# Kernel optimization log

Hardware: AMD Instinct MI355X
Metric: run time of the kernel (lower is better)

Reference implementation:

```python
import jax, jax.numpy as jnp
import numpy as np

N_NODES = 50000
N_EDGES = 800000
NODE_DIM = 64
EDGE_DIM = 16
HID = 64
HEADS = 4
LAYERS = 3
N_GRAPHS = 32
N_QUERY = 4096
BN_EPS = 1e-5
LRELU_SLOPE = 0.2


def setup_inputs() -> dict:
    key = jax.random.key(0)
    ks = jax.random.split(key, 20)
    s = 0.1  # weight scale
    return {
        "node_feat": jax.random.normal(ks[0], (N_NODES, NODE_DIM), jnp.float32),
        "edge_feat": jax.random.normal(ks[1], (N_EDGES, EDGE_DIM), jnp.float32),
        "node_proj_w": jax.random.normal(ks[2], (NODE_DIM, HID), jnp.float32) * s,
        "node_proj_b": jax.random.normal(ks[3], (HID,), jnp.float32) * s,
        "edge_proj_w": jax.random.normal(ks[4], (EDGE_DIM, HID), jnp.float32) * s,
        "edge_proj_b": jax.random.normal(ks[5], (HID,), jnp.float32) * s,
        "fc_w": jax.random.normal(ks[6], (LAYERS, HID, HEADS * HID), jnp.float32) * s,
        "fc_edge_w": jax.random.normal(ks[7], (LAYERS, HID, HEADS * HID), jnp.float32) * s,
        "attn_l": jax.random.normal(ks[8], (LAYERS, HEADS, HID), jnp.float32) * s,
        "attn_r": jax.random.normal(ks[9], (LAYERS, HEADS, HID), jnp.float32) * s,
        "attn_e": jax.random.normal(ks[10], (LAYERS, HEADS, HID), jnp.float32) * s,
        "conv_bias": jax.random.normal(ks[11], (LAYERS, HEADS * HID), jnp.float32) * s,
        "bn_gamma": jnp.ones((LAYERS, HID), jnp.float32),
        "bn_beta": jnp.zeros((LAYERS, HID), jnp.float32),
        "head_w": jax.random.normal(ks[12], (HEADS * HID, HID), jnp.float32) * s,
        "head_b": jax.random.normal(ks[13], (HID,), jnp.float32) * s,
        "src": jax.random.randint(ks[14], (N_EDGES,), 0, N_NODES, jnp.int64 if jax.config.jax_enable_x64 else jnp.int32),
        "dst": jax.random.randint(ks[15], (N_EDGES,), 0, N_NODES, jnp.int64 if jax.config.jax_enable_x64 else jnp.int32),
        "graph_ids": jnp.sort(jax.random.randint(ks[16], (N_NODES,), 0, N_GRAPHS)),
        "nodes_idx": jax.random.randint(ks[17], (N_QUERY,), 0, N_NODES),
        "num_graphs": N_GRAPHS,
    }


def reference(node_feat, edge_feat, node_proj_w, node_proj_b, edge_proj_w,
              edge_proj_b, fc_w, fc_edge_w, attn_l, attn_r, attn_e, conv_bias,
              bn_gamma, bn_beta, head_w, head_b, src, dst, graph_ids,
              nodes_idx, num_graphs):
    N = node_feat.shape[0]
    L, H, D = attn_l.shape

    nodes = node_feat @ node_proj_w + node_proj_b        # (N, hid)
    edges = edge_feat @ edge_proj_w + edge_proj_b        # (E, hid)

    x = None
    for l in range(L):
        # NOTE: faithful to original -- every layer consumes the ORIGINAL
        # projected node features (output is never fed back into `nodes`).
        ft = (nodes @ fc_w[l]).reshape(N, H, D)          # (N, H, D)
        fe = (edges @ fc_edge_w[l]).reshape(-1, H, D)    # (E, H, D)
        el = jnp.einsum('nhd,hd->nh', ft, attn_l[l])     # (N, H)
        er = jnp.einsum('nhd,hd->nh', ft, attn_r[l])
        ee = jnp.einsum('ehd,hd->eh', fe, attn_e[l])     # (E, H)
        e = jax.nn.leaky_relu(el[src] + er[dst] + ee, LRELU_SLOPE)
        # edge softmax over incoming edges of each destination node
        emax = jax.ops.segment_max(e, dst, num_segments=N)
        ex = jnp.exp(e - emax[dst])
        denom = jax.ops.segment_sum(ex, dst, num_segments=N)
        a = ex / denom[dst]                              # (E, H)
        # message = a * (feat_src + feat_edge), scatter-sum to dst
        m = a[:, :, None] * (ft[src] + fe)               # (E, H, D)
        rst = jax.ops.segment_sum(m, dst, num_segments=N)  # (N, H, D)
        rst = jax.nn.silu(rst + conv_bias[l].reshape(H, D))
        # BatchNorm1d(hidden) after permute(0,2,1): channel dim is D,
        # stats over (N, H). Training-mode batch statistics.
        mean = rst.mean(axis=(0, 1))
        var = rst.var(axis=(0, 1))
        x = (rst - mean) * jax.lax.rsqrt(var + BN_EPS) * bn_gamma[l] + bn_beta[l]

    x = x.reshape(N, H * D) @ head_w + head_b            # (N, hid)

    ones = jnp.ones((N, 1), x.dtype)
    sums = jax.ops.segment_sum(x, graph_ids, num_segments=num_graphs)
    counts = jax.ops.segment_sum(ones, graph_ids, num_segments=num_graphs)
    pooled = sums / jnp.maximum(counts, 1.0)             # (G, hid)
    return pooled, x[nodes_idx]
```

## Files before the change

### kernel.cpp

```cpp
#include <hip/hip_runtime.h>
#include <cstdint>
#include <cstddef>

#define N_NODES 50000
#define N_EDGES 800000
#define HID 64
#define HEADS 4
#define N_GRAPHS 32
#define N_QUERY 4096
#define N_TILES 3125
#define N_CWAVES 1563
#define N_CBLK 391
#define N_SBLK 49

typedef unsigned short ushort_t;
typedef unsigned int uint_t;
typedef __attribute__((ext_vector_type(8))) short short8_t;
typedef __attribute__((ext_vector_type(4))) float f32x4_t;

__device__ __forceinline__ float b2f(ushort_t h) { return __uint_as_float(((uint_t)h) << 16); }
__device__ __forceinline__ ushort_t f2b(float f) {
    uint_t u = __float_as_uint(f);
    uint_t r = (u + 0x7FFFu + ((u >> 16) & 1u)) >> 16;
    return (ushort_t)r;
}

static constexpr size_t OFF_DEG   = 0;
static constexpr size_t OFF_GST   = 50016;
static constexpr size_t OFF_OFFS  = 50064;
static constexpr size_t OFF_RANK  = 100080;
static constexpr size_t OFF_AL    = 900080;
static constexpr size_t OFF_AR    = 900336;
static constexpr size_t OFF_B     = 900592;
static constexpr size_t OFF_CE    = 900656;
static constexpr size_t OFF_CB    = 900672;
static constexpr size_t OFF_SS    = 900928;
static constexpr size_t OFF_HB2   = 901056;
static constexpr size_t OFF_WQE   = 901120;
static constexpr size_t OFF_WCVT  = 905216;
static constexpr size_t OFF_WHT   = 946176;
static constexpr size_t OFF_EL    = 954368;
static constexpr size_t OFF_ER    = 1154368;
static constexpr size_t OFF_NB    = 1354368;
static constexpr size_t OFF_REC   = 2954368;
static constexpr size_t OFF_U     = 6154624;
static constexpr size_t OFF_RST   = 14154624;
static constexpr size_t OFF_X     = 20554624;
static constexpr size_t OFF_SCR   = 23754624;
static constexpr size_t OFF_SCR2  = 24154624;
static constexpr size_t OFF_BSUM  = 24171008;
static constexpr size_t WS_TOTAL  = 24171072;

__global__ void setup1_kernel(const float* __restrict__ fcw2, const float* __restrict__ fcew2,
                              const float* __restrict__ attl2, const float* __restrict__ attr2,
                              const float* __restrict__ atte2,
                              const float* __restrict__ wpe, const float* __restrict__ bpe,
                              const int* __restrict__ gids,
                              float* __restrict__ Al, float* __restrict__ Ar,
                              float* __restrict__ B, float* __restrict__ Ce,
                              float* __restrict__ Cb, float* __restrict__ Wqe,
                              int* __restrict__ gstart)
{
    int b = blockIdx.x, tid = threadIdx.x;
    if (b == 0) {
        __shared__ float AE[256];
        int c = tid >> 2, h = tid & 3;
        float al = 0.f, ar = 0.f, ae = 0.f;
        for (int d = 0; d < 64; d++) {
            float wl = fcw2[c*256 + h*64 + d];
            float we = fcew2[c*256 + h*64 + d];
            al = fmaf(wl, attl2[h*64 + d], al);
            ar = fmaf(wl, attr2[h*64 + d], ar);
            ae = fmaf(we, atte2[h*64 + d], ae);
        }
        Al[c*4 + h] = al;
        Ar[c*4 + h] = ar;
        AE[c*4 + h] = ae;
        __syncthreads();
        if (tid < 64) {
            int kk = tid >> 2, hh = tid & 3;
            float bb = 0.f;
            for (int d = 0; d < 64; d++) bb = fmaf(wpe[kk*64 + d], AE[d*4 + hh], bb);
            B[kk*4 + hh] = bb;
        }
        if (tid < 4) {
            float ce = 0.f;
            for (int d = 0; d < 64; d++) ce = fmaf(bpe[d], AE[d*4 + tid], ce);
            Ce[tid] = ce;
        }
        {
            float cb = 0.f;
            for (int d = 0; d < 64; d++) cb = fmaf(bpe[d], fcew2[d*256 + tid], cb);
            Cb[tid] = cb;
        }
    } else if (b <= 16) {
        int idx = (b - 1) * 256 + tid;
        int hh = idx >> 10, rem = idx & 1023, kk = rem >> 6, cc = rem & 63;
        float w = 0.f;
        for (int d = 0; d < 64; d++) w = fmaf(wpe[kk*64 + d], fcew2[d*256 + hh*64 + cc], w);
        Wqe[idx] = w;
    } else {
        int g = tid;
        if (g <= N_GRAPHS) {
            int lo = 0, hi = N_NODES;
            while (lo < hi) { int mid = (lo + hi) >> 1; if (gids[mid] < g) lo = mid + 1; else hi = mid; }
            gstart[g] = lo;
        }
    }
}

__global__ void wcvt_kernel(const float* __restrict__ fcw2, const float* __restrict__ Wqe,
                            ushort_t* __restrict__ wcvt)
{
    int idx = blockIdx.x * 256 + threadIdx.x;
    int kt = idx >> 8, col = idx & 255;
    int hc = col >> 6;
    short8_t v8;
#pragma unroll
    for (int j = 0; j < 8; j++) {
        int k = kt*8 + j;
        float v;
        if (k < 256) {
            v = ((k >> 6) == hc) ? fcw2[(size_t)(k & 63)*256 + col] : 0.f;
        } else {
            int kq = k - 256, hh = kq >> 4;
            v = (hh == hc) ? Wqe[hh*1024 + (kq & 15)*64 + (col & 63)] : 0.f;
        }
        v8[j] = (short)f2b(v);
    }
    *(short8_t*)&wcvt[(size_t)idx*8] = v8;
}

__global__ __launch_bounds__(256) void node_proj_kernel(
    const float* __restrict__ nf, const float* __restrict__ wp, const float* __restrict__ bpn,
    const float* __restrict__ Al, const float* __restrict__ Ar,
    ushort_t* __restrict__ nb, float* __restrict__ el, float* __restrict__ er)
{
    __shared__ float rows[4][64];
    int tid = threadIdx.x, w = tid >> 6, lane = tid & 63;
    int n = blockIdx.x * 4 + w;
    rows[w][lane] = nf[(size_t)n*64 + lane];
    __syncthreads();
    float acc = bpn[lane];
    for (int k = 0; k < 64; k++) acc = fmaf(rows[w][k], wp[k*64 + lane], acc);
    nb[(size_t)n*64 + lane] = f2b(acc);
    float pl[4], pr[4];
#pragma unroll
    for (int h = 0; h < 4; h++) { pl[h] = acc * Al[lane*4 + h]; pr[h] = acc * Ar[lane*4 + h]; }
#pragma unroll
    for (int off = 32; off > 0; off >>= 1) {
#pragma unroll
        for (int h = 0; h < 4; h++) {
            pl[h] += __shfl_xor(pl[h], off, 64);
            pr[h] += __shfl_xor(pr[h], off, 64);
        }
    }
    if (lane == 0) {
#pragma unroll
        for (int h = 0; h < 4; h++) { el[(size_t)n*4 + h] = pl[h]; er[(size_t)n*4 + h] = pr[h]; }
    }
}

__global__ void hist_kernel(const int* __restrict__ dst, int* __restrict__ deg,
                            int* __restrict__ rank)
{
    int e = blockIdx.x * 256 + threadIdx.x;
    if (e < N_EDGES) rank[e] = atomicAdd(&deg[dst[e]], 1);
}

__global__ __launch_bounds__(1024) void scan1_kernel(const int* __restrict__ deg,
                                                     int* __restrict__ offs,
                                                     int* __restrict__ bsum)
{
    __shared__ int wsum[16];
    int b = blockIdx.x, tid = threadIdx.x, lane = tid & 63, w = tid >> 6;
    int i = b * 1024 + tid;
    int v = (i < N_NODES) ? deg[i] : 0;
    int incl = v;
#pragma unroll
    for (int off = 1; off < 64; off <<= 1) {
        int y = __shfl_up(incl, off, 64);
        if (lane >= off) incl += y;
    }
    if (lane == 63) wsum[w] = incl;
    __syncthreads();
    int woff = 0;
#pragma unroll
    for (int k = 0; k < 15; k++) woff += (k < w) ? wsum[k] : 0;
    if (i < N_NODES) offs[i] = woff + incl - v;
    if (tid == 1023) bsum[b] = woff + incl;
}

__global__ void scan2_kernel(int* __restrict__ bsum, int* __restrict__ offs)
{
    int tid = threadIdx.x;
    int v = (tid < N_SBLK) ? bsum[tid] : 0;
    int incl = v;
#pragma unroll
    for (int off = 1; off < 64; off <<= 1) {
        int y = __shfl_up(incl, off, 64);
        if (tid >= off) incl += y;
    }
    if (tid < N_SBLK) bsum[tid] = incl - v;
    if (tid == N_SBLK - 1) offs[N_NODES] = incl;
}

__global__ __launch_bounds__(1024) void scan3_kernel(int* __restrict__ offs,
                                                     const int* __restrict__ bsum)
{
    int i = blockIdx.x * 1024 + threadIdx.x;
    if (i < N_NODES) offs[i] += bsum[blockIdx.x];
}

__global__ __launch_bounds__(256) void logit_kernel(
    const int* __restrict__ rank, const int* __restrict__ offs,
    const int* __restrict__ src, const int* __restrict__ dst,
    const float* __restrict__ edge_feat, const float* __restrict__ el,
    const float* __restrict__ B, const float* __restrict__ Ce,
    int4* __restrict__ rec)
{
    int e = blockIdx.x * 256 + threadIdx.x;
    if (e >= N_EDGES) return;
    int sn = src[e], dn = dst[e];
    const float4* el4 = (const float4*)el;
    float4 a = el4[sn];
    float l0 = Ce[0] + a.x;
    float l1 = Ce[1] + a.y;
    float l2 = Ce[2] + a.z;
    float l3 = Ce[3] + a.w;
    const float4* ef4 = (const float4*)(edge_feat + (size_t)e * 16);
    float4 e0 = ef4[0], e1 = ef4[1], e2 = ef4[2], e3 = ef4[3];
    float ef[16] = {e0.x,e0.y,e0.z,e0.w, e1.x,e1.y,e1.z,e1.w,
                    e2.x,e2.y,e2.z,e2.w, e3.x,e3.y,e3.z,e3.w};
#pragma unroll
    for (int k = 0; k < 16; k++) {
        float f = ef[k];
        l0 = fmaf(f, B[k*4 + 0], l0);
        l1 = fmaf(f, B[k*4 + 1], l1);
        l2 = fmaf(f, B[k*4 + 2], l2);
        l3 = fmaf(f, B[k*4 + 3], l3);
    }
    int slot = offs[dn] + rank[e];
    uint_t lo01 = (uint_t)f2b(l0) | ((uint_t)f2b(l1) << 16);
    uint_t lo23 = (uint_t)f2b(l2) | ((uint_t)f2b(l3) << 16);
    rec[slot] = make_int4((int)lo01, (int)lo23, sn, e);
}

__global__ __launch_bounds__(256) void accum_kernel(
    const int* __restrict__ offs, const int4* __restrict__ rec,
    const float* __restrict__ er, const float* __restrict__ edge_feat,
    const ushort_t* __restrict__ nb, ushort_t* __restrict__ u)
{
    int tid = threadIdx.x;
    int lane = tid & 63;
    int li = lane & 15;
    int node = blockIdx.x * 16 + (tid >> 6) * 4 + ((lane >> 4) & 3);
    int start = offs[node], end = offs[node + 1];
    int deg = end - start;

    float4 er4 = *(const float4*)&er[(size_t)node*4];
    const int4 Z4 = make_int4(0, 0, 0, 0);
    int4 r0 = (li < deg)      ? rec[start + li]      : Z4;
    int4 r1 = (16 + li < deg) ? rec[start + 16 + li] : Z4;

    float pe0[4], pe1[4];
    {
        float l[4] = { b2f((ushort_t)((uint_t)r0.x & 0xffff)) + er4.x,
                       b2f((ushort_t)((uint_t)r0.x >> 16))    + er4.y,
                       b2f((ushort_t)((uint_t)r0.y & 0xffff)) + er4.z,
                       b2f((ushort_t)((uint_t)r0.y >> 16))    + er4.w };
#pragma unroll
        for (int h = 0; h < 4; h++) {
            float lv = (l[h] > 0.f) ? l[h] : 0.2f * l[h];
            pe0[h] = (li < deg) ? __expf(lv) : 0.f;
        }
    }
    {
        float l[4] = { b2f((ushort_t)((uint_t)r1.x & 0xffff)) + er4.x,
                       b2f((ushort_t)((uint_t)r1.x >> 16))    + er4.y,
                       b2f((ushort_t)((uint_t)r1.y & 0xffff)) + er4.z,
                       b2f((ushort_t)((uint_t)r1.y >> 16))    + er4.w };
#pragma unroll
        for (int h = 0; h < 4; h++) {
            float lv = (l[h] > 0.f) ? l[h] : 0.2f * l[h];
            pe1[h] = (16 + li < deg) ? __expf(lv) : 0.f;
        }
    }
    int sn0 = r0.z, eid0 = r0.w;
    int sn1 = r1.z, eid1 = r1.w;

    int mdeg = deg;
#pragma unroll
    for (int off = 1; off < 64; off <<= 1) mdeg = max(mdeg, __shfl_xor(mdeg, off, 64));
    mdeg = __builtin_amdgcn_readfirstlane(mdeg);

    float z0 = 0.f, z1 = 0.f, z2 = 0.f, z3 = 0.f;
    float t[4][4] = {{0.f}};
    float q[4] = {0.f, 0.f, 0.f, 0.f};
    int grpbase = lane & 48;

#pragma unroll 2
    for (int j = 0; j < mdeg; ++j) {
        bool act = j < deg;
        float a0, a1, a2, a3;
        int sn, eid;
        if (j < 32) {
            float v0 = (j < 16) ? pe0[0] : pe1[0];
            float v1 = (j < 16) ? pe0[1] : pe1[1];
            float v2 = (j < 16) ? pe0[2] : pe1[2];
            float v3 = (j < 16) ? pe0[3] : pe1[3];
            int vs = (j < 16) ? sn0 : sn1;
            int ve = (j < 16) ? eid0 : eid1;
            int sl = grpbase | (j & 15);
            a0 = __shfl(v0, sl, 64);
            a1 = __shfl(v1, sl, 64);
            a2 = __shfl(v2, sl, 64);
            a3 = __shfl(v3, sl, 64);
            sn  = __shfl(vs, sl, 64);
            eid = __shfl(ve, sl, 64);
        } else {
            a0 = a1 = a2 = a3 = 0.f;
            sn = 0; eid = 0;
            if (act) {
                int4 rr = rec[start + j];
                float l0 = b2f((ushort_t)((uint_t)rr.x & 0xffff)) + er4.x;
                float l1 = b2f((ushort_t)((uint_t)rr.x >> 16))    + er4.y;
                float l2 = b2f((ushort_t)((uint_t)rr.y & 0xffff)) + er4.z;
                float l3 = b2f((ushort_t)((uint_t)rr.y >> 16))    + er4.w;
                l0 = (l0 > 0.f) ? l0 : 0.2f * l0;
                l1 = (l1 > 0.f) ? l1 : 0.2f * l1;
                l2 = (l2 > 0.f) ? l2 : 0.2f * l2;
                l3 = (l3 > 0.f) ? l3 : 0.2f * l3;
                a0 = __expf(l0); a1 = __expf(l1); a2 = __expf(l2); a3 = __expf(l3);
                sn = rr.z; eid = rr.w;
            }
        }
        z0 += a0; z1 += a1; z2 += a2; z3 += a3;
        ushort4 nv = *(const ushort4*)&nb[(size_t)sn*64 + li*4];
        float nd0 = b2f(nv.x), nd1 = b2f(nv.y), nd2 = b2f(nv.z), nd3 = b2f(nv.w);
        t[0][0] = fmaf(a0, nd0, t[0][0]); t[0][1] = fmaf(a0, nd1, t[0][1]);
        t[0][2] = fmaf(a0, nd2, t[0][2]); t[0][3] = fmaf(a0, nd3, t[0][3]);
        t[1][0] = fmaf(a1, nd0, t[1][0]); t[1][1] = fmaf(a1, nd1, t[1][1]);
        t[1][2] = fmaf(a1, nd2, t[1][2]); t[1][3] = fmaf(a1, nd3, t[1][3]);
        t[2][0] = fmaf(a2, nd0, t[2][0]); t[2][1] = fmaf(a2, nd1, t[2][1]);
        t[2][2] = fmaf(a2, nd2, t[2][2]); t[2][3] = fmaf(a2, nd3, t[2][3]);
        t[3][0] = fmaf(a3, nd0, t[3][0]); t[3][1] = fmaf(a3, nd1, t[3][1]);
        t[3][2] = fmaf(a3, nd2, t[3][2]); t[3][3] = fmaf(a3, nd3, t[3][3]);
        float efv = edge_feat[(size_t)eid*16 + li];
        q[0] = fmaf(a0, efv, q[0]);
        q[1] = fmaf(a1, efv, q[1]);
        q[2] = fmaf(a2, efv, q[2]);
        q[3] = fmaf(a3, efv, q[3]);
    }

    float zinv[4];
    zinv[0] = (z0 > 0.f) ? 1.f / z0 : 0.f;
    zinv[1] = (z1 > 0.f) ? 1.f / z1 : 0.f;
    zinv[2] = (z2 > 0.f) ? 1.f / z2 : 0.f;
    zinv[3] = (z3 > 0.f) ? 1.f / z3 : 0.f;

    ushort_t* up = u + (size_t)node * 320;
#pragma unroll
    for (int h = 0; h < 4; h++) {
        ushort4 tv;
        tv.x = f2b(t[h][0] * zinv[h]); tv.y = f2b(t[h][1] * zinv[h]);
        tv.z = f2b(t[h][2] * zinv[h]); tv.w = f2b(t[h][3] * zinv[h]);
        *(ushort4*)&up[h*64 + li*4] = tv;
        up[256 + h*16 + li] = f2b(q[h] * zinv[h]);
    }
}

__global__ __launch_bounds__(256) void conv_kernel(
    const ushort_t* __restrict__ u, const ushort_t* __restrict__ wcvt,
    const float* __restrict__ Cb, const float* __restrict__ convb2,
    const int* __restrict__ offs, ushort_t* __restrict__ rst, float* __restrict__ scr)
{
    int tid = threadIdx.x, lane = tid & 63;
    int li = lane & 15, lg = lane >> 4;
    int widx = blockIdx.x * 4 + (tid >> 6);
    if (widx >= N_CWAVES) return;
    int tile0 = widx * 2, tile1 = widx * 2 + 1;
    bool t1ok = tile1 < N_TILES;
    int n0 = tile0 * 16;
    int n1 = t1ok ? tile1 * 16 : n0;

    short8_t a0[10], a1[10];
    const ushort_t* urow0 = u + (size_t)(n0 + li) * 320 + lg * 8;
    const ushort_t* urow1 = u + (size_t)(n1 + li) * 320 + lg * 8;
#pragma unroll
    for (int kt = 0; kt < 10; kt++) {
        a0[kt] = *(const short8_t*)(urow0 + kt * 32);
        a1[kt] = *(const short8_t*)(urow1 + kt * 32);
    }

    float fl0[4], fl1[4];
#pragma unroll
    for (int j = 0; j < 4; j++) {
        int na = n0 + lg*4 + j;
        int nbb = n1 + lg*4 + j;
        fl0[j] = (offs[na+1] > offs[na]) ? 1.f : 0.f;
        fl1[j] = (offs[nbb+1] > offs[nbb]) ? 1.f : 0.f;
    }

    const ushort_t* wbase = wcvt + ((size_t)lg * 256 + li) * 8;
    float ds[4] = {0.f, 0.f, 0.f, 0.f};
    float dsq[4] = {0.f, 0.f, 0.f, 0.f};

#pragma unroll 2
    for (int cb = 0; cb < 16; cb++) {
        short8_t b[10];
#pragma unroll
        for (int kt = 0; kt < 10; kt++)
            b[kt] = *(const short8_t*)(wbase + (size_t)kt * 8192 + (size_t)cb * 128);
        f32x4_t acc0 = (f32x4_t){0.f, 0.f, 0.f, 0.f};
        f32x4_t acc1 = (f32x4_t){0.f, 0.f, 0.f, 0.f};
#pragma unroll
        for (int kt = 0; kt < 10; kt++) {
            acc0 = __builtin_amdgcn_mfma_f32_16x16x32_bf16(a0[kt], b[kt], acc0, 0, 0, 0);
            acc1 = __builtin_amdgcn_mfma_f32_16x16x32_bf16(a1[kt], b[kt], acc1, 0, 0, 0);
        }
        int col = cb*16 + li;
        float bias = convb2[col];
        float cbv  = Cb[col];
        float s = 0.f, sq = 0.f;
#pragma unroll
        for (int j = 0; j < 4; j++) {
            float v = acc0[j] + bias + fl0[j] * cbv;
            float r = v / (1.f + __expf(-v));
            rst[(size_t)(n0 + lg*4 + j)*256 + col] = f2b(r);
            s += r; sq += r * r;
        }
        if (t1ok) {
#pragma unroll
            for (int j = 0; j < 4; j++) {
                float v = acc1[j] + bias + fl1[j] * cbv;
                float r = v / (1.f + __expf(-v));
                rst[(size_t)(n1 + lg*4 + j)*256 + col] = f2b(r);
                s += r; sq += r * r;
            }
        }
        s  += __shfl_xor(s, 16, 64);  s  += __shfl_xor(s, 32, 64);
        sq += __shfl_xor(sq, 16, 64); sq += __shfl_xor(sq, 32, 64);
        ds[cb & 3]  += s;
        dsq[cb & 3] += sq;
    }
    if (lg == 0) {
        float* sp = scr + (size_t)widx * 128;
#pragma unroll
        for (int m = 0; m < 4; m++) {
            sp[m*16 + li]      = ds[m];
            sp[64 + m*16 + li] = dsq[m];
        }
    }
}

__global__ __launch_bounds__(128) void scr_reduce_kernel(const float* __restrict__ scr,
                                                         float* __restrict__ scr2)
{
    int b = blockIdx.x, tid = threadIdx.x;
    float s = 0.f;
    for (int r = b; r < N_CWAVES; r += 128) s += scr[(size_t)r*128 + tid];
    scr2[(size_t)b*128 + tid] = s;
}

__global__ void bn_finalize_kernel(const float* __restrict__ scr2, const float* __restrict__ gamma2,
                                   const float* __restrict__ beta2, float* __restrict__ ss)
{
    __shared__ float part[8][128];
    __shared__ float tot[128];
    int j = threadIdx.x & 127, chunk = threadIdx.x >> 7;
    float t = 0.f;
    for (int b = chunk; b < 128; b += 8) t += scr2[(size_t)b*128 + j];
    part[chunk][j] = t;
    __syncthreads();
    if (threadIdx.x < 128) {
        float sgm = 0.f;
        for (int c = 0; c < 8; c++) sgm += part[c][threadIdx.x];
        tot[threadIdx.x] = sgm;
    }
    __syncthreads();
    if (threadIdx.x < 64) {
        float inv = 1.f / (float)(N_NODES * HEADS);
        float mean = tot[threadIdx.x] * inv;
        float var  = tot[64 + threadIdx.x] * inv - mean * mean;
        float sc = gamma2[threadIdx.x] * rsqrtf(var + 1e-5f);
        ss[threadIdx.x]      = sc;
        ss[64 + threadIdx.x] = beta2[threadIdx.x] - mean * sc;
    }
}

__global__ void head_prep_kernel(const float* __restrict__ ss, const float* __restrict__ headw,
                                 const float* __restrict__ headb,
                                 ushort_t* __restrict__ wht, float* __restrict__ hb2)
{
    int b = blockIdx.x, tid = threadIdx.x;
    if (b < 64) {
        int idx = b * 256 + tid;
        int c = idx >> 8, k = idx & 255;
        wht[(size_t)((k >> 3)*64 + c)*8 + (k & 7)] = f2b(ss[k & 63] * headw[(size_t)k*64 + c]);
    } else if (tid < 64) {
        float s = headb[tid];
        for (int k = 0; k < 256; k++) s += ss[64 + (k & 63)] * headw[(size_t)k*64 + tid];
        hb2[tid] = s;
    }
}

__global__ __launch_bounds__(512) void head_kernel(
    const ushort_t* __restrict__ rst, const ushort_t* __restrict__ wht,
    const float* __restrict__ hb2, float* __restrict__ x)
{
    __shared__ ushort_t Bs[16384];
    int tid = threadIdx.x, w = tid >> 6, lane = tid & 63;
    int li = lane & 15, lg = lane >> 4;
    int tile = blockIdx.x * 8 + w;
    bool active = tile < N_TILES;
    int n0 = tile * 16;

#pragma unroll
    for (int s = 0; s < 4; s++) {
        int i = tid + s*512;
        *(short8_t*)&Bs[(size_t)i*8] = *(const short8_t*)(wht + (size_t)i*8);
    }
    __syncthreads();

    if (!active) return;
    f32x4_t acc[4];
#pragma unroll
    for (int cb = 0; cb < 4; cb++) acc[cb] = (f32x4_t){0.f, 0.f, 0.f, 0.f};
    const ushort_t* rrow = rst + (size_t)(n0 + li) * 256 + lg * 8;
#pragma unroll
    for (int kt = 0; kt < 8; kt++) {
        short8_t a = *(const short8_t*)(rrow + kt * 32);
        short8_t b[4];
#pragma unroll
        for (int cb = 0; cb < 4; cb++)
            b[cb] = *(const short8_t*)&Bs[(size_t)((kt*4 + lg)*64 + cb*16 + li)*8];
#pragma unroll
        for (int cb = 0; cb < 4; cb++)
            acc[cb] = __builtin_amdgcn_mfma_f32_16x16x32_bf16(a, b[cb], acc[cb], 0, 0, 0);
    }
#pragma unroll
    for (int cb = 0; cb < 4; cb++) {
        int col = cb*16 + li;
        float hb = hb2[col];
#pragma unroll
        for (int j = 0; j < 4; j++)
            x[(size_t)(n0 + lg*4 + j)*64 + col] = acc[cb][j] + hb;
    }
}

__global__ __launch_bounds__(1024) void pool_kernel(const float* __restrict__ x,
                                                    const int* __restrict__ gstart,
                                                    float* __restrict__ out)
{
    __shared__ float red[16][64];
    int g = blockIdx.x;
    int lane = threadIdx.x & 63, w = threadIdx.x >> 6;
    int s = gstart[g], e = gstart[g + 1];
    float acc = 0.f;
    for (int n = s + w; n < e; n += 16) acc += x[(size_t)n*64 + lane];
    red[w][lane] = acc;
    __syncthreads();
    if (w == 0) {
        float t = 0.f;
#pragma unroll
        for (int k = 0; k < 16; k++) t += red[k][lane];
        float c = (float)(e - s);
        out[(size_t)g*64 + lane] = t / fmaxf(c, 1.f);
    }
}

__global__ void gather_kernel(const float* __restrict__ x, const int* __restrict__ nidx,
                              float* __restrict__ outq)
{
    int i = blockIdx.x * 256 + threadIdx.x;
    if (i < N_QUERY * HID) {
        int q = i >> 6, c = i & 63;
        outq[i] = x[(size_t)nidx[q]*64 + c];
    }
}

extern "C" void kernel_launch(void* const* d_in, const int* in_sizes, int n_in,
                              void* d_out, int out_size, void* d_ws, size_t ws_size,
                              hipStream_t stream)
{
    const float* node_feat   = (const float*)d_in[0];
    const float* edge_feat   = (const float*)d_in[1];
    const float* node_proj_w = (const float*)d_in[2];
    const float* node_proj_b = (const float*)d_in[3];
    const float* edge_proj_w = (const float*)d_in[4];
    const float* edge_proj_b = (const float*)d_in[5];
    const float* fc_w        = (const float*)d_in[6];
    const float* fc_edge_w   = (const float*)d_in[7];
    const float* attn_l      = (const float*)d_in[8];
    const float* attn_r      = (const float*)d_in[9];
    const float* attn_e      = (const float*)d_in[10];
    const float* conv_bias   = (const float*)d_in[11];
    const float* bn_gamma    = (const float*)d_in[12];
    const float* bn_beta     = (const float*)d_in[13];
    const float* head_w      = (const float*)d_in[14];
    const float* head_b      = (const float*)d_in[15];
    const int*   src         = (const int*)d_in[16];
    const int*   dst         = (const int*)d_in[17];
    const int*   gids        = (const int*)d_in[18];
    const int*   nidx        = (const int*)d_in[19];

    if (ws_size < WS_TOTAL * sizeof(float)) return;

    float* ws  = (float*)d_ws;
    float* out = (float*)d_out;

    const int L2 = 2;
    const float* fcw2   = fc_w      + (size_t)L2 * HID * HEADS * HID;
    const float* fcew2  = fc_edge_w + (size_t)L2 * HID * HEADS * HID;
    const float* attl2  = attn_l    + (size_t)L2 * HEADS * HID;
    const float* attr2  = attn_r    + (size_t)L2 * HEADS * HID;
    const float* atte2  = attn_e    + (size_t)L2 * HEADS * HID;
    const float* convb2 = conv_bias + (size_t)L2 * HEADS * HID;
    const float* gamma2 = bn_gamma  + (size_t)L2 * HID;
    const float* beta2  = bn_beta   + (size_t)L2 * HID;

    int*   deg     = (int*)(ws + OFF_DEG);
    int*   gstart  = (int*)(ws + OFF_GST);
    int*   offs    = (int*)(ws + OFF_OFFS);
    int*   rank    = (int*)(ws + OFF_RANK);
    float* Al      = ws + OFF_AL;
    float* Ar      = ws + OFF_AR;
    float* Bm      = ws + OFF_B;
    float* Ce      = ws + OFF_CE;
    float* Cb      = ws + OFF_CB;
    float* ss      = ws + OFF_SS;
    float* hb2     = ws + OFF_HB2;
    float* Wqe     = ws + OFF_WQE;
    ushort_t* wcvt = (ushort_t*)(ws + OFF_WCVT);
    ushort_t* wht  = (ushort_t*)(ws + OFF_WHT);
    float* el      = ws + OFF_EL;
    float* er      = ws + OFF_ER;
    ushort_t* nb   = (ushort_t*)(ws + OFF_NB);
    int4*  rec     = (int4*)(ws + OFF_REC);
    ushort_t* u    = (ushort_t*)(ws + OFF_U);
    ushort_t* rst  = (ushort_t*)(ws + OFF_RST);
    float* x       = ws + OFF_X;
    float* scr     = ws + OFF_SCR;
    float* scr2    = ws + OFF_SCR2;
    int*   bsum    = (int*)(ws + OFF_BSUM);

    hipMemsetAsync(d_ws, 0, N_NODES * sizeof(int), stream);

    setup1_kernel<<<18, 256, 0, stream>>>(fcw2, fcew2, attl2, attr2, atte2,
                                          edge_proj_w, edge_proj_b, gids,
                                          Al, Ar, Bm, Ce, Cb, Wqe, gstart);
    wcvt_kernel<<<40, 256, 0, stream>>>(fcw2, Wqe, wcvt);
    node_proj_kernel<<<N_NODES/4, 256, 0, stream>>>(node_feat, node_proj_w, node_proj_b,
                                                    Al, Ar, nb, el, er);
    hist_kernel<<<(N_EDGES + 255)/256, 256, 0, stream>>>(dst, deg, rank);
    scan1_kernel<<<N_SBLK, 1024, 0, stream>>>(deg, offs, bsum);
    scan2_kernel<<<1, 64, 0, stream>>>(bsum, offs);
    scan3_kernel<<<N_SBLK, 1024, 0, stream>>>(offs, bsum);
    logit_kernel<<<(N_EDGES + 255)/256, 256, 0, stream>>>(rank, offs, src, dst, edge_feat,
                                                          el, Bm, Ce, rec);
    accum_kernel<<<N_NODES/16, 256, 0, stream>>>(offs, rec, er, edge_feat, nb, u);
    conv_kernel<<<N_CBLK, 256, 0, stream>>>(u, wcvt, Cb, convb2, offs, rst, scr);
    scr_reduce_kernel<<<128, 128, 0, stream>>>(scr, scr2);
    bn_finalize_kernel<<<1, 1024, 0, stream>>>(scr2, gamma2, beta2, ss);
    head_prep_kernel<<<65, 256, 0, stream>>>(ss, head_w, head_b, wht, hb2);
    head_kernel<<<(N_TILES + 7)/8, 512, 0, stream>>>(rst, wht, hb2, x);
    pool_kernel<<<N_GRAPHS, 1024, 0, stream>>>(x, gstart, out);
    gather_kernel<<<(N_QUERY*HID + 255)/256, 256, 0, stream>>>(x, nidx, out + N_GRAPHS*HID);
}
```

Baseline: 252.8 us.

## Compute node projection with bf16 MFMA tiles instead of scalar FMA

```diff
diff --git a/kernel.cpp b/kernel.cpp
--- a/kernel.cpp
+++ b/kernel.cpp
@@ -12,6 +12,7 @@
 #define N_CWAVES 1563
 #define N_CBLK 391
 #define N_SBLK 49
+#define N_PBLK 782
 
 typedef unsigned short ushort_t;
 typedef unsigned int uint_t;
@@ -49,17 +50,18 @@
 static constexpr size_t OFF_SCR   = 23754624;
 static constexpr size_t OFF_SCR2  = 24154624;
 static constexpr size_t OFF_BSUM  = 24171008;
-static constexpr size_t WS_TOTAL  = 24171072;
+static constexpr size_t OFF_WPB   = 24171072;
+static constexpr size_t WS_TOTAL  = 24173120;
 
 __global__ void setup1_kernel(const float* __restrict__ fcw2, const float* __restrict__ fcew2,
                               const float* __restrict__ attl2, const float* __restrict__ attr2,
                               const float* __restrict__ atte2,
                               const float* __restrict__ wpe, const float* __restrict__ bpe,
-                              const int* __restrict__ gids,
+                              const float* __restrict__ wpn, const int* __restrict__ gids,
                               float* __restrict__ Al, float* __restrict__ Ar,
                               float* __restrict__ B, float* __restrict__ Ce,
                               float* __restrict__ Cb, float* __restrict__ Wqe,
-                              int* __restrict__ gstart)
+                              int* __restrict__ gstart, ushort_t* __restrict__ wpb)
 {
     int b = blockIdx.x, tid = threadIdx.x;
     if (b == 0) {
@@ -99,12 +101,22 @@
         float w = 0.f;
         for (int d = 0; d < 64; d++) w = fmaf(wpe[kk*64 + d], fcew2[d*256 + hh*64 + cc], w);
         Wqe[idx] = w;
-    } else {
+    } else if (b == 17) {
         int g = tid;
         if (g <= N_GRAPHS) {
             int lo = 0, hi = N_NODES;
             while (lo < hi) { int mid = (lo + hi) >> 1; if (gids[mid] < g) lo = mid + 1; else hi = mid; }
             gstart[g] = lo;
+        }
+    } else {
+        for (int s = 0; s < 2; s++) {
+            int g = tid + s*256;
+            int kt = g >> 8, lg = (g >> 6) & 3, cb = (g >> 4) & 3, li = g & 15;
+            short8_t v;
+#pragma unroll
+            for (int j = 0; j < 8; j++)
+                v[j] = (short)f2b(wpn[(size_t)(kt*32 + lg*8 + j)*64 + cb*16 + li]);
+            *(short8_t*)&wpb[(size_t)g*8] = v;
         }
     }
 }
@@ -132,32 +144,76 @@
 }
 
 __global__ __launch_bounds__(256) void node_proj_kernel(
-    const float* __restrict__ nf, const float* __restrict__ wp, const float* __restrict__ bpn,
-    const float* __restrict__ Al, const float* __restrict__ Ar,
+    const float* __restrict__ nf, const ushort_t* __restrict__ wpb,
+    const float* __restrict__ bpn, const float* __restrict__ Al, const float* __restrict__ Ar,
     ushort_t* __restrict__ nb, float* __restrict__ el, float* __restrict__ er)
 {
-    __shared__ float rows[4][64];
-    int tid = threadIdx.x, w = tid >> 6, lane = tid & 63;
-    int n = blockIdx.x * 4 + w;
-    rows[w][lane] = nf[(size_t)n*64 + lane];
-    __syncthreads();
-    float acc = bpn[lane];
-    for (int k = 0; k < 64; k++) acc = fmaf(rows[w][k], wp[k*64 + lane], acc);
-    nb[(size_t)n*64 + lane] = f2b(acc);
-    float pl[4], pr[4];
-#pragma unroll
-    for (int h = 0; h < 4; h++) { pl[h] = acc * Al[lane*4 + h]; pr[h] = acc * Ar[lane*4 + h]; }
-#pragma unroll
-    for (int off = 32; off > 0; off >>= 1) {
-#pragma unroll
-        for (int h = 0; h < 4; h++) {
-            pl[h] += __shfl_xor(pl[h], off, 64);
-            pr[h] += __shfl_xor(pr[h], off, 64);
-        }
-    }
-    if (lane == 0) {
-#pragma unroll
-        for (int h = 0; h < 4; h++) { el[(size_t)n*4 + h] = pl[h]; er[(size_t)n*4 + h] = pr[h]; }
+    int tid = threadIdx.x, lane = tid & 63;
+    int li = lane & 15, lg = lane >> 4;
+    int tile = blockIdx.x * 4 + (tid >> 6);
+    if (tile >= N_TILES) return;
+    int n0 = tile * 16;
+
+    short8_t a[2];
+#pragma unroll
+    for (int kt = 0; kt < 2; kt++) {
+        const float* ap = nf + (size_t)(n0 + li) * 64 + kt*32 + lg*8;
+        float4 f0 = *(const float4*)ap;
+        float4 f1 = *(const float4*)(ap + 4);
+        short8_t v;
+        v[0] = (short)f2b(f0.x); v[1] = (short)f2b(f0.y);
+        v[2] = (short)f2b(f0.z); v[3] = (short)f2b(f0.w);
+        v[4] = (short)f2b(f1.x); v[5] = (short)f2b(f1.y);
+        v[6] = (short)f2b(f1.z); v[7] = (short)f2b(f1.w);
+        a[kt] = v;
+    }
+
+    f32x4_t acc[4];
+#pragma unroll
+    for (int cb = 0; cb < 4; cb++) acc[cb] = (f32x4_t){0.f, 0.f, 0.f, 0.f};
+#pragma unroll
+    for (int kt = 0; kt < 2; kt++) {
+#pragma unroll
+        for (int cb = 0; cb < 4; cb++) {
+            short8_t b = *(const short8_t*)&wpb[(size_t)((((kt*4 + lg)*4 + cb)*16) + li)*8];
+            acc[cb] = __builtin_amdgcn_mfma_f32_16x16x32_bf16(a[kt], b, acc[cb], 0, 0, 0);
+        }
+    }
+
+    float pl[4][4] = {{0.f}}, pr[4][4] = {{0.f}};
+#pragma unroll
+    for (int cb = 0; cb < 4; cb++) {
+        int c = cb*16 + li;
+        float bias = bpn[c];
+#pragma unroll
+        for (int j = 0; j < 4; j++) {
+            float val = acc[cb][j] + bias;
+            nb[(size_t)(n0 + lg*4 + j)*64 + c] = f2b(val);
+#pragma unroll
+            for (int h = 0; h < 4; h++) {
+                pl[j][h] = fmaf(val, Al[c*4 + h], pl[j][h]);
+                pr[j][h] = fmaf(val, Ar[c*4 + h], pr[j][h]);
+            }
+        }
+    }
+#pragma unroll
+    for (int off = 1; off < 16; off <<= 1) {
+#pragma unroll
+        for (int j = 0; j < 4; j++)
+#pragma unroll
+            for (int h = 0; h < 4; h++) {
+                pl[j][h] += __shfl_xor(pl[j][h], off, 64);
+                pr[j][h] += __shfl_xor(pr[j][h], off, 64);
+            }
+    }
+    if (li < 4) {
+        int h = li;
+#pragma unroll
+        for (int j = 0; j < 4; j++) {
+            int n = n0 + lg*4 + j;
+            el[(size_t)n*4 + h] = pl[j][h];
+            er[(size_t)n*4 + h] = pr[j][h];
+        }
     }
 }
 
@@ -644,15 +700,16 @@
     float* scr     = ws + OFF_SCR;
     float* scr2    = ws + OFF_SCR2;
     int*   bsum    = (int*)(ws + OFF_BSUM);
+    ushort_t* wpb  = (ushort_t*)(ws + OFF_WPB);
 
     hipMemsetAsync(d_ws, 0, N_NODES * sizeof(int), stream);
 
-    setup1_kernel<<<18, 256, 0, stream>>>(fcw2, fcew2, attl2, attr2, atte2,
-                                          edge_proj_w, edge_proj_b, gids,
-                                          Al, Ar, Bm, Ce, Cb, Wqe, gstart);
+    setup1_kernel<<<19, 256, 0, stream>>>(fcw2, fcew2, attl2, attr2, atte2,
+                                          edge_proj_w, edge_proj_b, node_proj_w, gids,
+                                          Al, Ar, Bm, Ce, Cb, Wqe, gstart, wpb);
     wcvt_kernel<<<40, 256, 0, stream>>>(fcw2, Wqe, wcvt);
-    node_proj_kernel<<<N_NODES/4, 256, 0, stream>>>(node_feat, node_proj_w, node_proj_b,
-                                                    Al, Ar, nb, el, er);
+    node_proj_kernel<<<N_PBLK, 256, 0, stream>>>(node_feat, wpb, node_proj_b,
+                                                 Al, Ar, nb, el, er);
     hist_kernel<<<(N_EDGES + 255)/256, 256, 0, stream>>>(dst, deg, rank);
     scan1_kernel<<<N_SBLK, 1024, 0, stream>>>(deg, offs, bsum);
     scan2_kernel<<<1, 64, 0, stream>>>(bsum, offs);
```

New measurement: 249.7 us (median of 2 runs). No clear change (-1.2%).
